# Kernel optimization log

Hardware: AMD Instinct MI355X
Metric: run time of the kernel (lower is better)

The kernel has to match this reference:

```python
import jax, jax.numpy as jnp
import numpy as np

EMBED_DIM = 2048
HEAD_DIM = 128            # __init__ head_dim arg
HALF = HEAD_DIM // 2      # internal self.head_dim = 64
NH2 = EMBED_DIM // HALF   # 32 q/k heads
H = NH2 // 2              # 16 differential heads
DEPTH = 12
LAMBDA_INIT = 0.8 - 0.6 * float(np.exp(-0.3 * DEPTH))
SCALING = HEAD_DIM ** (-0.5)   # source divides scores by this (== *sqrt(head_dim))
BATCH, SEQ = 1, 2048
EPS = 1e-5


def setup_inputs() -> dict:
    key = jax.random.key(0)
    ks = jax.random.split(key, 10)
    wstd = 0.25 / float(np.sqrt(EMBED_DIM))  # keep logits moderate despite *sqrt(head_dim)
    return {
        "x": jax.random.normal(ks[0], (BATCH, SEQ, EMBED_DIM), jnp.float32),
        "wq": jax.random.normal(ks[1], (EMBED_DIM, EMBED_DIM), jnp.float32) * wstd,
        "wk": jax.random.normal(ks[2], (EMBED_DIM, EMBED_DIM), jnp.float32) * wstd,
        "wv": jax.random.normal(ks[3], (EMBED_DIM, EMBED_DIM), jnp.float32) * wstd,
        "wout": jax.random.normal(ks[4], (EMBED_DIM, EMBED_DIM), jnp.float32) * wstd,
        "lambda_q1": jax.random.normal(ks[5], (HALF,), jnp.float32) * 0.1,
        "lambda_q2": jax.random.normal(ks[6], (HALF,), jnp.float32) * 0.1,
        "lambda_k1": jax.random.normal(ks[7], (HALF,), jnp.float32) * 0.1,
        "lambda_k2": jax.random.normal(ks[8], (HALF,), jnp.float32) * 0.1,
        "subln_weight": jnp.ones((2 * HALF,), jnp.float32),
    }


def _rope_tables(t, dim):
    # precompute_freqs_cis: freqs = 1/theta^(arange(0,dim,2)/dim); angles = outer(t, freqs)
    inv = 1.0 / (10000.0 ** (np.arange(0, dim, 2)[: dim // 2].astype(np.float64) / dim))
    ang = np.outer(np.arange(t), inv)
    return jnp.asarray(np.cos(ang), jnp.float32), jnp.asarray(np.sin(ang), jnp.float32)


def _apply_rope(x, cos, sin):
    # x: [b, t, h, d]; interleaved (even, odd) pairs form complex numbers
    xr, xi = x[..., 0::2], x[..., 1::2]
    c = cos[None, :, None, :]
    s = sin[None, :, None, :]
    out = jnp.stack([xr * c - xi * s, xr * s + xi * c], axis=-1)
    return out.reshape(x.shape)


def reference(x, wq, wk, wv, wout, lambda_q1, lambda_q2, lambda_k1, lambda_k2, subln_weight):
    b, t, e = x.shape
    # nn.Linear(bias=False): y = x @ W^T
    q = (x @ wq.T).reshape(b, t, NH2, HALF)
    k = (x @ wk.T).reshape(b, t, NH2, HALF)
    v = (x @ wv.T).reshape(b, t, H, 2 * HALF)  # intended DIFF-attn layout
    cos, sin = _rope_tables(t, HALF)
    q = _apply_rope(q, cos, sin)
    k = _apply_rope(k, cos, sin)
    q = q.transpose(0, 2, 1, 3)  # [b, 2H, t, HALF]
    k = k.transpose(0, 2, 1, 3)
    v = v.transpose(0, 2, 1, 3)  # [b, H, t, 2*HALF]
    # source: attn_weights = qk / scaling  (scaling = head_dim**-0.5 -> multiply by sqrt(head_dim))
    scores = jnp.einsum('bhtd,bhsd->bhts', q, k) / SCALING
    # default attn_mask = triu(zeros) == all zeros -> no masking applied
    probs = jax.nn.softmax(scores, axis=-1)
    lam1 = jnp.exp(jnp.sum(lambda_q1 * lambda_k1))
    lam2 = jnp.exp(jnp.sum(lambda_q2 * lambda_k2))
    lam = lam1 - lam2 + LAMBDA_INIT
    probs = probs.reshape(b, H, 2, t, t)
    diff = probs[:, :, 0] - lam * probs[:, :, 1]        # [b, H, t, t]
    attn = jnp.einsum('bhts,bhsd->bhtd', diff, v)        # [b, H, t, 2*HALF]
    # RMSNorm(2*HALF, eps=1e-5)
    attn = attn * jax.lax.rsqrt(jnp.mean(attn * attn, axis=-1, keepdims=True) + EPS)
    attn = attn * subln_weight
    attn = attn.transpose(0, 2, 1, 3).reshape(b, t, e)
    return attn @ wout.T
```

## Files before the change

kernel.cpp:

```cpp
#include <hip/hip_runtime.h>
#include <math.h>

#define SEQ 2048
#define EMB 2048

typedef _Float16 f16;
typedef unsigned short ushort_t;
typedef __attribute__((ext_vector_type(2))) _Float16 f16x2;
typedef __attribute__((ext_vector_type(4))) _Float16 f16x4;
typedef __attribute__((ext_vector_type(8))) _Float16 f16x8;
typedef __attribute__((ext_vector_type(4))) float f32x4;
typedef __attribute__((ext_vector_type(16))) float f32x16;
typedef __attribute__((ext_vector_type(8))) short bf16x8;
typedef __attribute__((ext_vector_type(4))) unsigned short us4;
typedef __attribute__((ext_vector_type(8))) unsigned short us8;
typedef __attribute__((ext_vector_type(4))) unsigned int uint4v;

__device__ __forceinline__ void gload16(const void* g, void* l) {
  __builtin_amdgcn_global_load_lds((const __attribute__((address_space(1))) unsigned int*)g,
                                   (__attribute__((address_space(3))) unsigned int*)l, 16, 0, 0);
}

__device__ __forceinline__ ushort_t f32_to_bf16(float f) {
  unsigned int u = __builtin_bit_cast(unsigned int, f);
  u += 0x7FFFu + ((u >> 16) & 1u);
  return (ushort_t)(u >> 16);
}

__device__ __forceinline__ unsigned cvt_pk_bf16_2(float lo, float hi) {
  unsigned r;
  asm("v_cvt_pk_bf16_f32 %0, %1, %2" : "=v"(r) : "v"(lo), "v"(hi));
  return r;
}

__global__ __launch_bounds__(256) void cvt5_rope_kernel(
    const float* __restrict__ i0, const float* __restrict__ i1, const float* __restrict__ i2,
    const float* __restrict__ i3, const float* __restrict__ i4, f16* __restrict__ o0,
    f16* __restrict__ o1, f16* __restrict__ o2, f16* __restrict__ o3, f16* __restrict__ o4,
    float* __restrict__ cosT, float* __restrict__ sinT) {
  int b = blockIdx.x;
  if (b < 256) {
    int id = b * 256 + threadIdx.x;
    int t = id >> 5, i = id & 31;
    double inv = pow(10000.0, -(double)i / 32.0);
    double ang = (double)t * inv;
    cosT[id] = (float)cos(ang);
    sinT[id] = (float)sin(ang);
    return;
  }
  b -= 256;
  int z = b >> 12;
  const float* in = (z == 0) ? i0 : (z == 1) ? i1 : (z == 2) ? i2 : (z == 3) ? i3 : i4;
  f16* out = (z == 0) ? o0 : (z == 1) ? o1 : (z == 2) ? o2 : (z == 3) ? o3 : o4;
  int i = ((b & 4095) * 256 + threadIdx.x) * 4;
  f32x4 v = *(const f32x4*)(in + i);
  *(f16x4*)(out + i) = __builtin_convertvector(v, f16x4);
}

__global__ __launch_bounds__(256, 3) void proj_gemm_kernel(
    const f16* __restrict__ A, const f16* __restrict__ B0, const f16* __restrict__ B1,
    const f16* __restrict__ B2, const float* __restrict__ cosT, const float* __restrict__ sinT,
    f16* __restrict__ qout, f16* __restrict__ kout, ushort_t* __restrict__ vtout) {
  const int z = blockIdx.z;
  const f16* __restrict__ B = (z == 0) ? B0 : ((z == 1) ? B1 : B2);
  __shared__ f16 As[2][128 * 32];
  __shared__ f16 Bs[2][128 * 32];
  const int tid = threadIdx.x;
  const int wave = tid >> 6, lane = tid & 63;
  const int l16 = lane & 15, quad = lane >> 4;
  const int wm = (wave >> 1) << 6, wn = (wave & 1) << 6;
  const int bm = blockIdx.y << 7, bn = blockIdx.x << 7;

  const int swg = ((lane & 3) ^ ((lane >> 3) & 3)) * 8;
  const f16* Ag = A + (size_t)(bm + wave * 32 + (lane >> 2)) * EMB + swg;
  const f16* Bg = B + (size_t)(bn + wave * 32 + (lane >> 2)) * EMB + swg;
  const int sl = wave * 1024 + lane * 8;

  const int swr = (quad ^ ((l16 >> 1) & 3)) * 8;
  int aoff[4], boff[4];
#pragma unroll
  for (int i = 0; i < 4; i++) {
    aoff[i] = (wm + i * 16 + l16) * 32 + swr;
    boff[i] = (wn + i * 16 + l16) * 32 + swr;
  }

  f32x4 acc[4][4];
#pragma unroll
  for (int i = 0; i < 4; i++)
#pragma unroll
    for (int j = 0; j < 4; j++) acc[i][j] = (f32x4){0.f, 0.f, 0.f, 0.f};

  for (int k0 = 0; k0 < EMB; k0 += 64) {
    __syncthreads();
    gload16(Ag + k0, &As[0][sl]);
    gload16(Ag + (size_t)16 * EMB + k0, &As[0][sl + 512]);
    gload16(Ag + k0 + 32, &As[1][sl]);
    gload16(Ag + (size_t)16 * EMB + k0 + 32, &As[1][sl + 512]);
    gload16(Bg + k0, &Bs[0][sl]);
    gload16(Bg + (size_t)16 * EMB + k0, &Bs[0][sl + 512]);
    gload16(Bg + k0 + 32, &Bs[1][sl]);
    gload16(Bg + (size_t)16 * EMB + k0 + 32, &Bs[1][sl + 512]);
    __syncthreads();
#pragma unroll
    for (int g = 0; g < 2; g++) {
      f16x8 af[4], bf[4];
#pragma unroll
      for (int mi = 0; mi < 4; mi++) af[mi] = *(const f16x8*)&As[g][aoff[mi]];
#pragma unroll
      for (int ni = 0; ni < 4; ni++) bf[ni] = *(const f16x8*)&Bs[g][boff[ni]];
#pragma unroll
      for (int mi = 0; mi < 4; mi++)
#pragma unroll
        for (int ni = 0; ni < 4; ni++)
          acc[mi][ni] =
              __builtin_amdgcn_mfma_f32_16x16x32_f16(af[mi], bf[ni], acc[mi][ni], 0, 0, 0);
    }
  }

  if (z == 2) {
#pragma unroll
    for (int mi = 0; mi < 4; mi++) {
#pragma unroll
      for (int ni = 0; ni < 4; ni++) {
        int row0 = bm + wm + mi * 16 + quad * 4;
        int col = bn + wn + ni * 16 + l16;
        us4 o;
#pragma unroll
        for (int rg = 0; rg < 4; rg++) o[rg] = f32_to_bf16(acc[mi][ni][rg]);
        int hidx = col >> 7, d = col & 127, t = row0;
        size_t idx = ((((size_t)hidx * 32 + (t >> 6)) * 4 + ((t >> 4) & 3)) * 4 + (d >> 5)) * 512 +
                     (((t >> 3) & 1) * 32 + (d & 31)) * 8 + (t & 7);
        *(us4*)&vtout[idx] = o;
      }
    }
  } else {
    f16* Co = (z == 0) ? qout : kout;
    const float scale = (z == 0) ? 16.3222307f : 1.0f;
#pragma unroll
    for (int mi = 0; mi < 4; mi++) {
#pragma unroll
      for (int ni = 0; ni < 4; ni++) {
        int row0 = bm + wm + mi * 16 + quad * 4;
        int col = bn + wn + ni * 16 + l16;
        int i_r = (col & 63) >> 1;
        int odd = col & 1;
        int hidx = col >> 7, d = col & 127;
#pragma unroll
        for (int rg = 0; rg < 4; rg++) {
          int t = row0 + rg;
          float c = cosT[(t << 5) + i_r] * scale;
          float s = sinT[(t << 5) + i_r] * scale;
          float own = acc[mi][ni][rg];
          float other = __shfl_xor(own, 1);
          float xr = odd ? other : own;
          float xi = odd ? own : other;
          float outv = odd ? (xr * s + xi * c) : (xr * c - xi * s);
          size_t idx = ((size_t)((hidx * 64 + (t >> 5)) * 8 + (d >> 4))) * 512 +
                       ((t & 31) + ((d >> 3) & 1) * 32) * 8 + (d & 7);
          Co[idx] = (f16)outv;
        }
      }
    }
  }
}

__global__ __launch_bounds__(256, 2) void out_gemm_kernel(const f16* __restrict__ A,
                                                          const f16* __restrict__ B,
                                                          float* __restrict__ C) {
  __shared__ f16 As[2][128 * 32];
  __shared__ f16 Bs[2][64 * 32];
  const int tid = threadIdx.x;
  const int wave = tid >> 6, lane = tid & 63;
  const int l16 = lane & 15, quad = lane >> 4;
  const int wm = (wave >> 1) << 6, wn = (wave & 1) << 5;
  const int bm = blockIdx.y << 7, bn = blockIdx.x << 6;

  const int swg = ((lane & 3) ^ ((lane >> 3) & 3)) * 8;
  const f16* Ag = A + (size_t)(bm + wave * 32 + (lane >> 2)) * EMB + swg;
  const f16* Bg = B + (size_t)(bn + wave * 16 + (lane >> 2)) * EMB + swg;
  const int sla = wave * 1024 + lane * 8;
  const int slb = wave * 512 + lane * 8;

  const int swr = (quad ^ ((l16 >> 1) & 3)) * 8;
  int aoff[4], boff[2];
#pragma unroll
  for (int i = 0; i < 4; i++) aoff[i] = (wm + i * 16 + l16) * 32 + swr;
#pragma unroll
  for (int i = 0; i < 2; i++) boff[i] = (wn + i * 16 + l16) * 32 + swr;

  f32x4 acc[4][2];
#pragma unroll
  for (int i = 0; i < 4; i++)
#pragma unroll
    for (int j = 0; j < 2; j++) acc[i][j] = (f32x4){0.f, 0.f, 0.f, 0.f};

  for (int k0 = 0; k0 < EMB; k0 += 64) {
    __syncthreads();
    gload16(Ag + k0, &As[0][sla]);
    gload16(Ag + (size_t)16 * EMB + k0, &As[0][sla + 512]);
    gload16(Ag + k0 + 32, &As[1][sla]);
    gload16(Ag + (size_t)16 * EMB + k0 + 32, &As[1][sla + 512]);
    gload16(Bg + k0, &Bs[0][slb]);
    gload16(Bg + k0 + 32, &Bs[1][slb]);
    __syncthreads();
#pragma unroll
    for (int g = 0; g < 2; g++) {
      f16x8 af[4], bf[2];
#pragma unroll
      for (int mi = 0; mi < 4; mi++) af[mi] = *(const f16x8*)&As[g][aoff[mi]];
#pragma unroll
      for (int ni = 0; ni < 2; ni++) bf[ni] = *(const f16x8*)&Bs[g][boff[ni]];
#pragma unroll
      for (int mi = 0; mi < 4; mi++)
#pragma unroll
        for (int ni = 0; ni < 2; ni++)
          acc[mi][ni] =
              __builtin_amdgcn_mfma_f32_16x16x32_f16(af[mi], bf[ni], acc[mi][ni], 0, 0, 0);
    }
  }

#pragma unroll
  for (int mi = 0; mi < 4; mi++) {
#pragma unroll
    for (int ni = 0; ni < 2; ni++) {
      int row0 = bm + wm + mi * 16 + quad * 4;
      int col = bn + wn + ni * 16 + l16;
#pragma unroll
      for (int rg = 0; rg < 4; rg++)
        C[(size_t)(row0 + rg) * EMB + col] = acc[mi][ni][rg];
    }
  }
}

__global__ __launch_bounds__(256, 2) void diff_attn_v11(
    const f16* __restrict__ qbT, const f16* __restrict__ kbT, const ushort_t* __restrict__ vbT,
    const float* __restrict__ lq1, const float* __restrict__ lq2,
    const float* __restrict__ lk1, const float* __restrict__ lk2,
    const float* __restrict__ subw, f16* __restrict__ attnb) {
  const int h = blockIdx.x;
  const int qblk = blockIdx.y;
  const int tid = threadIdx.x;
  const int wave = tid >> 6, lane = tid & 63;
  const int l32 = lane & 31, hi = lane >> 5;
  const int hh = wave >> 1, qs = wave & 1;

  __shared__ float Obuf[8192];

  const int qrow0 = qblk * 64 + qs * 32;
  f16x8 qf[4];
  {
    const f16* qT = qbT + ((size_t)((h * 64 + qblk * 2 + qs) * 8 + hh * 4)) * 512 + lane * 8;
#pragma unroll
    for (int c = 0; c < 4; c++) qf[c] = *(const f16x8*)(qT + c * 512);
  }

  f32x16 O[4];
#pragma unroll
  for (int dt = 0; dt < 4; dt++)
#pragma unroll
    for (int s2 = 0; s2 < 16; s2++) O[dt][s2] = 0.f;
  float lsum = 0.f;

  const f16* kT = kbT + ((size_t)(h * 64) * 8 + hh * 4) * 512 + lane * 8;
  const ushort_t* vT = vbT + (size_t)h * 262144 + lane * 8;

  auto loadK = [&](f16x8(&kr)[4], int it) {
    const f16* p = kT + (size_t)it * 4096;
#pragma unroll
    for (int c = 0; c < 4; c++) kr[c] = *(const f16x8*)(p + c * 512);
  };
  auto loadV = [&](us8(&vr)[8], int it) {
    const ushort_t* p = vT + (size_t)it * 4096;
#pragma unroll
    for (int T = 0; T < 8; T++) vr[T] = *(const us8*)(p + T * 512);
  };

  auto compute = [&](const f16x8(&kr)[4], const us8(&vr)[8]) {
    f32x16 acc;
#pragma unroll
    for (int s2 = 0; s2 < 16; s2++) acc[s2] = -28.8539008f;
#pragma unroll
    for (int c = 0; c < 4; c++)
      acc = __builtin_amdgcn_mfma_f32_32x32x16_f16(kr[c], qf[c], acc, 0, 0, 0);
    float p[16];
#pragma unroll
    for (int s2 = 0; s2 < 16; s2++) p[s2] = __builtin_exp2f(acc[s2]);
    lsum += (((p[0] + p[1]) + (p[2] + p[3])) + ((p[4] + p[5]) + (p[6] + p[7]))) +
            (((p[8] + p[9]) + (p[10] + p[11])) + ((p[12] + p[13]) + (p[14] + p[15])));
    bf16x8 pf[2];
#pragma unroll
    for (int c2 = 0; c2 < 2; c2++) {
      unsigned w0 = cvt_pk_bf16_2(p[8 * c2 + 0], p[8 * c2 + 1]);
      unsigned w1 = cvt_pk_bf16_2(p[8 * c2 + 2], p[8 * c2 + 3]);
      unsigned w2 = cvt_pk_bf16_2(p[8 * c2 + 4], p[8 * c2 + 5]);
      unsigned w3 = cvt_pk_bf16_2(p[8 * c2 + 6], p[8 * c2 + 7]);
      asm("v_permlane32_swap_b32 %0, %1" : "+v"(w0), "+v"(w2));
      asm("v_permlane32_swap_b32 %0, %1" : "+v"(w1), "+v"(w3));
      uint4v pw;
      pw.x = w0; pw.y = w1; pw.z = w2; pw.w = w3;
      pf[c2] = __builtin_bit_cast(bf16x8, pw);
    }
    __builtin_amdgcn_s_setprio(1);
#pragma unroll
    for (int c2 = 0; c2 < 2; c2++) {
#pragma unroll
      for (int dt = 0; dt < 4; dt++) {
        bf16x8 vf = __builtin_bit_cast(bf16x8, vr[c2 * 4 + dt]);
        O[dt] = __builtin_amdgcn_mfma_f32_32x32x16_bf16(vf, pf[c2], O[dt], 0, 0, 0);
      }
    }
    __builtin_amdgcn_s_setprio(0);
  };

  f16x8 kA[4], kB[4];
  us8 vA[8], vB[8];
  loadK(kA, 0);
  loadV(vA, 0);
  loadK(kB, 1);
  loadV(vB, 1);
  for (int it = 0; it < 64; it += 2) {
    compute(kA, vA);
    if (it + 2 < 64) {
      loadK(kA, it + 2);
      loadV(vA, it + 2);
    }
    compute(kB, vB);
    if (it + 3 < 64) {
      loadK(kB, it + 3);
      loadV(vB, it + 3);
    }
  }

  float d1 = 0.f, d2 = 0.f;
  for (int i = 0; i < 64; i++) {
    d1 += lq1[i] * lk1[i];
    d2 += lq2[i] * lk2[i];
  }
  const float lam = __expf(d1) - __expf(d2) + 0.783605767f;

  float s = lsum + __shfl_xor(lsum, 32);
  const float inv = (hh == 0) ? (1.f / s) : (lam / s);

  if (hh == 1) {
#pragma unroll
    for (int dt = 0; dt < 4; dt++)
#pragma unroll
      for (int rq = 0; rq < 4; rq++) {
        f32x4 v;
#pragma unroll
        for (int rg = 0; rg < 4; rg++) v[rg] = O[dt][rq * 4 + rg] * inv;
        *(f32x4*)&Obuf[(((qs * 4 + dt) * 4 + rq) * 64 + lane) * 4] = v;
      }
  }
  __syncthreads();
  if (hh == 0) {
    float a[4][16];
    float ms = 0.f;
#pragma unroll
    for (int dt = 0; dt < 4; dt++)
#pragma unroll
      for (int rq = 0; rq < 4; rq++) {
        f32x4 o1 = *(const f32x4*)&Obuf[(((qs * 4 + dt) * 4 + rq) * 64 + lane) * 4];
#pragma unroll
        for (int rg = 0; rg < 4; rg++) {
          float v = O[dt][rq * 4 + rg] * inv - o1[rg];
          a[dt][rq * 4 + rg] = v;
          ms += v * v;
        }
      }
    ms += __shfl_xor(ms, 32);
    const float rms = rsqrtf(ms * (1.f / 128.f) + 1e-5f);
    const int t_g = qrow0 + l32;
#pragma unroll
    for (int dt = 0; dt < 4; dt++)
#pragma unroll
      for (int rq = 0; rq < 4; rq++) {
        f32x4 sw = *(const f32x4*)(subw + dt * 32 + rq * 8 + hi * 4);
        f16x4 o;
#pragma unroll
        for (int rg = 0; rg < 4; rg++) o[rg] = (f16)(a[dt][rq * 4 + rg] * rms * sw[rg]);
        *(f16x4*)(attnb + (size_t)t_g * EMB + h * 128 + dt * 32 + rq * 8 + hi * 4) = o;
      }
  }
}

extern "C" void kernel_launch(void* const* d_in, const int* in_sizes, int n_in,
                              void* d_out, int out_size, void* d_ws, size_t ws_size,
                              hipStream_t stream) {
  const float* x    = (const float*)d_in[0];
  const float* wq   = (const float*)d_in[1];
  const float* wk   = (const float*)d_in[2];
  const float* wv   = (const float*)d_in[3];
  const float* wout = (const float*)d_in[4];
  const float* lq1  = (const float*)d_in[5];
  const float* lq2  = (const float*)d_in[6];
  const float* lk1  = (const float*)d_in[7];
  const float* lk2  = (const float*)d_in[8];
  const float* subw = (const float*)d_in[9];
  float* out = (float*)d_out;

  char* ws = (char*)d_ws;
  const size_t MB = 1024 * 1024;
  f16* xb    = (f16*)(ws + 0 * MB);
  f16* wqb   = (f16*)(ws + 8 * MB);
  f16* wkb   = (f16*)(ws + 16 * MB);
  f16* wvb   = (f16*)(ws + 24 * MB);
  f16* woutb = (f16*)(ws + 32 * MB);
  f16* qbT   = (f16*)(ws + 40 * MB);
  f16* kbT   = (f16*)(ws + 48 * MB);
  ushort_t* vbT = (ushort_t*)(ws + 56 * MB);
  f16* attnb = (f16*)(ws + 64 * MB);
  float* cosT = (float*)(ws + 72 * MB);
  float* sinT = (float*)(ws + 72 * MB + 262144);

  dim3 b256(256);
  cvt5_rope_kernel<<<5 * 4096 + 256, b256, 0, stream>>>(x, wq, wk, wv, wout, xb, wqb, wkb, wvb,
                                                        woutb, cosT, sinT);

  proj_gemm_kernel<<<dim3(16, 16, 3), b256, 0, stream>>>(xb, wqb, wkb, wvb, cosT, sinT, qbT, kbT,
                                                         vbT);

  diff_attn_v11<<<dim3(16, 32), b256, 0, stream>>>(qbT, kbT, vbT, lq1, lq2, lk1, lk2, subw,
                                                   attnb);

  out_gemm_kernel<<<dim3(32, 16), b256, 0, stream>>>(attnb, woutb, out);
}
```

Measured before the change: 288.9 us.

## Split attention KV range across waves and double the query-block grid

Each block now handles 32 query rows instead of 64, and its two wave pairs split the key/value sequence (interleaved tiles) instead of splitting query rows. Partial softmax sums and outputs are combined through shared memory before the differential subtraction and RMSNorm. The grid doubles to 1024 blocks, which gives more parallelism across CUs. In exchange, each K/V tile is loaded by twice as many blocks in total, and the epilogue gains extra shared-memory reductions and barriers.

Result: slower. 297.2 us (+2.9%).

```diff
diff --git a/kernel.cpp b/kernel.cpp
--- a/kernel.cpp
+++ b/kernel.cpp
@@ -232,7 +232,7 @@
   }
 }
 
-__global__ __launch_bounds__(256, 2) void diff_attn_v11(
+__global__ __launch_bounds__(256, 2) void diff_attn_v16(
     const f16* __restrict__ qbT, const f16* __restrict__ kbT, const ushort_t* __restrict__ vbT,
     const float* __restrict__ lq1, const float* __restrict__ lq2,
     const float* __restrict__ lk1, const float* __restrict__ lk2,
@@ -242,14 +242,15 @@
   const int tid = threadIdx.x;
   const int wave = tid >> 6, lane = tid & 63;
   const int l32 = lane & 31, hi = lane >> 5;
-  const int hh = wave >> 1, qs = wave & 1;
-
-  __shared__ float Obuf[8192];
-
-  const int qrow0 = qblk * 64 + qs * 32;
+  const int hh = wave >> 1, ks = wave & 1;
+
+  __shared__ float OB[8192];
+  __shared__ float lsb[2][2][32];
+
+  const int qrow0 = qblk * 32;
   f16x8 qf[4];
   {
-    const f16* qT = qbT + ((size_t)((h * 64 + qblk * 2 + qs) * 8 + hh * 4)) * 512 + lane * 8;
+    const f16* qT = qbT + ((size_t)((h * 64 + qblk) * 8 + hh * 4)) * 512 + lane * 8;
 #pragma unroll
     for (int c = 0; c < 4; c++) qf[c] = *(const f16x8*)(qT + c * 512);
   }
@@ -314,20 +315,20 @@
 
   f16x8 kA[4], kB[4];
   us8 vA[8], vB[8];
-  loadK(kA, 0);
-  loadV(vA, 0);
-  loadK(kB, 1);
-  loadV(vB, 1);
-  for (int it = 0; it < 64; it += 2) {
+  loadK(kA, ks);
+  loadV(vA, ks);
+  loadK(kB, ks + 2);
+  loadV(vB, ks + 2);
+  for (int si = 0; si < 32; si += 2) {
     compute(kA, vA);
-    if (it + 2 < 64) {
-      loadK(kA, it + 2);
-      loadV(vA, it + 2);
+    if (si + 2 < 32) {
+      loadK(kA, ks + 2 * (si + 2));
+      loadV(vA, ks + 2 * (si + 2));
     }
     compute(kB, vB);
-    if (it + 3 < 64) {
-      loadK(kB, it + 3);
-      loadV(vB, it + 3);
+    if (si + 3 < 32) {
+      loadK(kB, ks + 2 * (si + 3));
+      loadV(vB, ks + 2 * (si + 3));
     }
   }
 
@@ -338,32 +339,65 @@
   }
   const float lam = __expf(d1) - __expf(d2) + 0.783605767f;
 
-  float s = lsum + __shfl_xor(lsum, 32);
-  const float inv = (hh == 0) ? (1.f / s) : (lam / s);
-
-  if (hh == 1) {
+  const float sp = lsum + __shfl_xor(lsum, 32);
+  if (hi == 0) lsb[hh][ks][l32] = sp;
+  __syncthreads();
+  const float den = lsb[hh][0][l32] + lsb[hh][1][l32];
+  const float inv = (hh == 0) ? (1.f / den) : (lam / den);
+
+#pragma unroll
+  for (int dt = 0; dt < 4; dt++)
+#pragma unroll
+    for (int s2 = 0; s2 < 16; s2++) O[dt][s2] *= inv;
+
+  auto obIdx = [&](int hhR, int dt, int rq) { return (((hhR * 4 + dt) * 4 + rq) * 64 + lane) * 4; };
+
+  if (ks == 1) {
 #pragma unroll
     for (int dt = 0; dt < 4; dt++)
 #pragma unroll
       for (int rq = 0; rq < 4; rq++) {
         f32x4 v;
 #pragma unroll
-        for (int rg = 0; rg < 4; rg++) v[rg] = O[dt][rq * 4 + rg] * inv;
-        *(f32x4*)&Obuf[(((qs * 4 + dt) * 4 + rq) * 64 + lane) * 4] = v;
+        for (int rg = 0; rg < 4; rg++) v[rg] = O[dt][rq * 4 + rg];
+        *(f32x4*)&OB[obIdx(hh, dt, rq)] = v;
       }
   }
   __syncthreads();
-  if (hh == 0) {
+  if (ks == 0) {
+#pragma unroll
+    for (int dt = 0; dt < 4; dt++)
+#pragma unroll
+      for (int rq = 0; rq < 4; rq++) {
+        f32x4 v1 = *(const f32x4*)&OB[obIdx(hh, dt, rq)];
+#pragma unroll
+        for (int rg = 0; rg < 4; rg++) O[dt][rq * 4 + rg] += v1[rg];
+      }
+  }
+  __syncthreads();
+  if (ks == 0 && hh == 1) {
+#pragma unroll
+    for (int dt = 0; dt < 4; dt++)
+#pragma unroll
+      for (int rq = 0; rq < 4; rq++) {
+        f32x4 v;
+#pragma unroll
+        for (int rg = 0; rg < 4; rg++) v[rg] = O[dt][rq * 4 + rg];
+        *(f32x4*)&OB[obIdx(1, dt, rq)] = v;
+      }
+  }
+  __syncthreads();
+  if (ks == 0 && hh == 0) {
     float a[4][16];
     float ms = 0.f;
 #pragma unroll
     for (int dt = 0; dt < 4; dt++)
 #pragma unroll
       for (int rq = 0; rq < 4; rq++) {
-        f32x4 o1 = *(const f32x4*)&Obuf[(((qs * 4 + dt) * 4 + rq) * 64 + lane) * 4];
+        f32x4 o1 = *(const f32x4*)&OB[obIdx(1, dt, rq)];
 #pragma unroll
         for (int rg = 0; rg < 4; rg++) {
-          float v = O[dt][rq * 4 + rg] * inv - o1[rg];
+          float v = O[dt][rq * 4 + rg] - o1[rg];
           a[dt][rq * 4 + rg] = v;
           ms += v * v;
         }
@@ -420,7 +454,7 @@
   proj_gemm_kernel<<<dim3(16, 16, 3), b256, 0, stream>>>(xb, wqb, wkb, wvb, cosT, sinT, qbT, kbT,
                                                          vbT);
 
-  diff_attn_v11<<<dim3(16, 32), b256, 0, stream>>>(qbT, kbT, vbT, lq1, lq2, lk1, lk2, subw,
+  diff_attn_v16<<<dim3(16, 64), b256, 0, stream>>>(qbT, kbT, vbT, lq1, lq2, lk1, lk2, subw,
                                                    attnb);
 
   out_gemm_kernel<<<dim3(32, 16), b256, 0, stream>>>(attnb, woutb, out);
```
